# Optimization experiments

Hardware: AMD Instinct MI355X
Metric: run time of the kernel (lower is better)

The kernel has to match this reference:

```python
import jax, jax.numpy as jnp
import numpy as np

B = 4          # batch (number of point clouds)
NPER = 50000   # voxels per cloud
G = 96         # voxel grid extent per axis
C = 128        # in_channels
R = 2          # reduction_ratio
K = 27         # 3^3 kernel offsets
BN_EPS = 1e-5


def _build_sparse_geometry(seed=0):
    """Unique voxel coords per sample + 27-neighbor kernel map (Minkowski-style)."""
    rng = np.random.default_rng(seed)
    keys_list = []
    for b in range(B):
        loc = rng.choice(G ** 3, NPER, replace=False)
        loc.sort()
        keys_list.append(b * (G ** 3) + loc)
    keys = np.concatenate(keys_list)  # globally sorted (batch-major)
    N = keys.shape[0]
    loc = keys % (G ** 3)
    xs, ys, zs = loc // (G * G), (loc // G) % G, loc % G
    offsets = [(dx, dy, dz) for dx in (-1, 0, 1) for dy in (-1, 0, 1) for dz in (-1, 0, 1)]
    nbr_idx = np.zeros((N, K), np.int32)
    nbr_mask = np.zeros((N, K), bool)
    for k, (dx, dy, dz) in enumerate(offsets):
        inb = ((xs + dx >= 0) & (xs + dx < G) & (ys + dy >= 0) & (ys + dy < G)
               & (zs + dz >= 0) & (zs + dz < G))
        nkey = keys + dx * G * G + dy * G + dz
        pos = np.searchsorted(keys, nkey)
        pos_c = np.clip(pos, 0, N - 1)
        found = inb & (keys[pos_c] == nkey)
        nbr_idx[:, k] = np.where(found, pos_c, 0)
        nbr_mask[:, k] = found
    batch_idx = np.repeat(np.arange(B), NPER).astype(np.int32)
    return nbr_idx, nbr_mask, batch_idx


def setup_inputs() -> dict:
    nbr_idx, nbr_mask, batch_idx = _build_sparse_geometry(0)
    N = B * NPER
    key = jax.random.key(0)
    ks = jax.random.split(key, 8)
    feats = jax.random.normal(ks[0], (N, C), jnp.float32)
    # channel-attention MLP (MinkowskiLinear has bias=True)
    w1 = jax.random.normal(ks[1], (C, C // R), jnp.float32) * (1.0 / np.sqrt(C))
    b1 = jnp.zeros((C // R,), jnp.float32)
    w2 = jax.random.normal(ks[2], (C // R, C), jnp.float32) * (1.0 / np.sqrt(C // R))
    b2 = jnp.zeros((C,), jnp.float32)
    # spatial attention: 3x3x3 sparse conv C->4 (bias=False), BN(4), 1x1x1 conv 4->4
    conv1_w = jax.random.normal(ks[3], (K, C, 4), jnp.float32) * (1.0 / np.sqrt(K * C))
    bn_gamma = jnp.ones((4,), jnp.float32)
    bn_beta = jnp.zeros((4,), jnp.float32)
    conv2_w = jax.random.normal(ks[4], (4, 4), jnp.float32) * 0.5
    return dict(feats=feats, w1=w1, b1=b1, w2=w2, b2=b2, conv1_w=conv1_w,
                bn_gamma=bn_gamma, bn_beta=bn_beta, conv2_w=conv2_w,
                nbr_idx=jnp.asarray(nbr_idx), nbr_mask=jnp.asarray(nbr_mask),
                batch_idx=jnp.asarray(batch_idx), num_batches=B)


def reference(feats, w1, b1, w2, b2, conv1_w, bn_gamma, bn_beta, conv2_w,
              nbr_idx, nbr_mask, batch_idx, num_batches):
    N = feats.shape[0]
    ones = jnp.ones((N,), feats.dtype)
    counts = jax.ops.segment_sum(ones, batch_idx, num_segments=num_batches,
                                 indices_are_sorted=True)  # [B]
    avg_x = jax.ops.segment_sum(feats, batch_idx, num_segments=num_batches,
                                indices_are_sorted=True) / counts[:, None]  # [B,C]
    max_x = jax.ops.segment_max(feats, batch_idx, num_segments=num_batches,
                                indices_are_sorted=True)  # [B,C]
    mlp = lambda z: jax.nn.relu(z @ w1 + b1) @ w2 + b2
    weights = jax.nn.sigmoid(mlp(avg_x) + mlp(max_x))  # [B,C] channel attention
    # sam_mid: per-sample broadcast multiply
    mid = feats * weights[batch_idx]  # [N,C]
    # sparse 3x3x3 conv C->4 via kernel map (gather + thin matmul per offset)
    mask_f = nbr_mask.astype(feats.dtype)
    y = jnp.zeros((N, 4), feats.dtype)
    for k in range(K):
        y = y + (mid[nbr_idx[:, k]] * mask_f[:, k:k + 1]) @ conv1_w[k]
    # BatchNorm (training-mode batch stats, biased var) + ReLU
    mu = jnp.mean(y, axis=0)
    var = jnp.var(y, axis=0)
    y = (y - mu) * jax.lax.rsqrt(var + BN_EPS) * bn_gamma + bn_beta
    y = jax.nn.relu(y)
    # 1x1x1 conv == linear (bias=False), then sigmoid
    final = jax.nn.sigmoid(y @ conv2_w)  # [N,4]
    # sam_output: max over channels -> scalar spatial gate per point
    gate = jnp.max(final, axis=1, keepdims=True)  # [N,1]
    out = mid * gate + mid + feats
    return out
```

## Files before the change

kernel.cpp:

```cpp
#include <hip/hip_runtime.h>

#define C 128
#define K 27
#define BATCHES 4
#define RA_BPB 512
#define CONV_BLOCKS 512
#define CONV_TPB 1024
#define NWAVES_CONV (CONV_BLOCKS * (CONV_TPB / 64))
#define BN_EPS 1e-5f

typedef __attribute__((ext_vector_type(2))) __fp16 h2;
typedef __attribute__((ext_vector_type(8))) __fp16 h8;

__global__ __launch_bounds__(256) void reduceA_kernel(
    const float* __restrict__ feats, float* __restrict__ psum,
    float* __restrict__ pmax, const unsigned int* __restrict__ mwords,
    int* __restrict__ flag, int NPER) {
  int base = blockIdx.x * 512;
  bool bad = false;
  bad |= (mwords[base + threadIdx.x] > 1u);
  bad |= (mwords[base + 256 + threadIdx.x] > 1u);
  if (__any(bad) && (threadIdx.x & 63) == 0) atomicOr(flag, 1);

  int b = blockIdx.x / RA_BPB, chunk = blockIdx.x % RA_BPB;
  int CH = (NPER + RA_BPB - 1) / RA_BPB;
  int r0 = b * NPER + chunk * CH;
  int r1 = min(b * NPER + NPER, r0 + CH);
  int g = threadIdx.x >> 5;
  int l = threadIdx.x & 31;
  float4 s = make_float4(0.f, 0.f, 0.f, 0.f);
  float4 m = make_float4(-INFINITY, -INFINITY, -INFINITY, -INFINITY);
  int i = r0 + g;
  for (; i + 8 < r1; i += 16) {
    float4 v1 = *(const float4*)(feats + (size_t)i * C + l * 4);
    float4 v2 = *(const float4*)(feats + (size_t)(i + 8) * C + l * 4);
    s.x += v1.x + v2.x; s.y += v1.y + v2.y;
    s.z += v1.z + v2.z; s.w += v1.w + v2.w;
    m.x = fmaxf(m.x, fmaxf(v1.x, v2.x)); m.y = fmaxf(m.y, fmaxf(v1.y, v2.y));
    m.z = fmaxf(m.z, fmaxf(v1.z, v2.z)); m.w = fmaxf(m.w, fmaxf(v1.w, v2.w));
  }
  if (i < r1) {
    float4 v = *(const float4*)(feats + (size_t)i * C + l * 4);
    s.x += v.x; s.y += v.y; s.z += v.z; s.w += v.w;
    m.x = fmaxf(m.x, v.x); m.y = fmaxf(m.y, v.y);
    m.z = fmaxf(m.z, v.z); m.w = fmaxf(m.w, v.w);
  }
  __shared__ float ssum[8][C], smax[8][C];
  *(float4*)&ssum[g][l * 4] = s;
  *(float4*)&smax[g][l * 4] = m;
  __syncthreads();
  if (threadIdx.x < C) {
    int c = threadIdx.x;
    float S = 0.f, M = -INFINITY;
#pragma unroll
    for (int gg = 0; gg < 8; ++gg) {
      S += ssum[gg][c];
      M = fmaxf(M, smax[gg][c]);
    }
    psum[(size_t)blockIdx.x * C + c] = S;
    pmax[(size_t)blockIdx.x * C + c] = M;
  }
}

__global__ __launch_bounds__(256) void reduceB_kernel(
    const float* __restrict__ psum, const float* __restrict__ pmax,
    float* __restrict__ avg, float* __restrict__ mx, int NPER) {
  int b = blockIdx.x;
  int g = threadIdx.x >> 5, l = threadIdx.x & 31;
  float4 s = make_float4(0.f, 0.f, 0.f, 0.f);
  float4 m = make_float4(-INFINITY, -INFINITY, -INFINITY, -INFINITY);
  for (int j = g; j < RA_BPB; j += 8) {
    size_t base = (size_t)(b * RA_BPB + j) * C + l * 4;
    float4 vs = *(const float4*)(psum + base);
    float4 vm = *(const float4*)(pmax + base);
    s.x += vs.x; s.y += vs.y; s.z += vs.z; s.w += vs.w;
    m.x = fmaxf(m.x, vm.x); m.y = fmaxf(m.y, vm.y);
    m.z = fmaxf(m.z, vm.z); m.w = fmaxf(m.w, vm.w);
  }
  __shared__ float ssum[8][C], smax[8][C];
  *(float4*)&ssum[g][l * 4] = s;
  *(float4*)&smax[g][l * 4] = m;
  __syncthreads();
  if (threadIdx.x < C) {
    int c = threadIdx.x;
    float S = 0.f, M = -INFINITY;
#pragma unroll
    for (int gg = 0; gg < 8; ++gg) {
      S += ssum[gg][c];
      M = fmaxf(M, smax[gg][c]);
    }
    avg[b * C + c] = S / (float)NPER;
    mx[b * C + c] = M;
  }
}

__global__ void mlp_kernel(const float* __restrict__ avg, const float* __restrict__ mx,
                           const float* __restrict__ w1, const float* __restrict__ b1,
                           const float* __restrict__ w2, const float* __restrict__ b2,
                           float* __restrict__ wgt) {
  int b = blockIdx.x, t = threadIdx.x;
  __shared__ float h1a[64], h1m[64];
  if (t < 64) {
    float sa = b1[t], sm = b1[t];
    for (int c = 0; c < C; ++c) {
      float wv = w1[c * 64 + t];
      sa += avg[b * C + c] * wv;
      sm += mx[b * C + c] * wv;
    }
    h1a[t] = fmaxf(sa, 0.f);
    h1m[t] = fmaxf(sm, 0.f);
  }
  __syncthreads();
  float za = b2[t], zm = b2[t];
  for (int h = 0; h < 64; ++h) {
    float wv = w2[h * C + t];
    za += h1a[h] * wv;
    zm += h1m[h] * wv;
  }
  float z = za + zm;
  wgt[b * C + t] = 1.f / (1.f + expf(-z));
}

__global__ __launch_bounds__(CONV_TPB, 8) void conv_kernel(
    const float* __restrict__ feats, const float* __restrict__ wgt,
    const float* __restrict__ conv1_w, const int* __restrict__ nbr_idx,
    const void* __restrict__ nbr_mask, const int* __restrict__ flagp,
    float* __restrict__ y, float* __restrict__ bnpart, int N, int NPER) {
  __shared__ __align__(16) h8 wlds[K * 64];
  int tid = threadIdx.x;
  for (int e = tid; e < K * 64; e += CONV_TPB) {
    float4 A = ((const float4*)conv1_w)[e * 2];
    float4 B = ((const float4*)conv1_w)[e * 2 + 1];
    h8 w;
    h2 p;
    p = __builtin_amdgcn_cvt_pkrtz(A.x, B.x); w[0] = p[0]; w[1] = p[1];
    p = __builtin_amdgcn_cvt_pkrtz(A.y, B.y); w[2] = p[0]; w[3] = p[1];
    p = __builtin_amdgcn_cvt_pkrtz(A.z, B.z); w[4] = p[0]; w[5] = p[1];
    p = __builtin_amdgcn_cvt_pkrtz(A.w, B.w); w[6] = p[0]; w[7] = p[1];
    wlds[e] = w;
  }
  __syncthreads();

  int lane = tid & 63;
  int g = lane >> 4, cl = lane & 15;
  int gwave = blockIdx.x * (CONV_TPB / 64) + (tid >> 6);
  int nwaves = gridDim.x * (CONV_TPB / 64);
  int rpw = (N + nwaves - 1) / nwaves;
  int rbeg = gwave * rpw, rend = min(N, rbeg + rpw);
  bool byteMode = (*flagp != 0);
  const unsigned char* mb = (const unsigned char*)nbr_mask;
  const int* mi = (const int*)nbr_mask;

  int bB = min(rbeg / NPER, BATCHES - 1);
  int bEnd = (bB + 1) * NPER;
  float2 wr = *(const float2*)(wgt + bB * C + 2 * lane);

  bool mk = false;
  int jl = 0;
  if (rbeg < rend && lane < K) {
    size_t e = (size_t)rbeg * K + lane;
    mk = byteMode ? (mb[e] != 0) : (mi[e] != 0);
    jl = nbr_idx[e];
  }

  float sAcc = 0.f, qAcc = 0.f;

  unsigned balTailN = 0, balTailP = 0;
  int jN = 0, jP = 0, cntN = 0, cntP = 0;
  int k0N = 0, k1N = 0, k2N = 0, k3N = 0, k0P = 0, k1P = 0, k2P = 0, k3P = 0;
  float2 g0N = make_float2(0, 0), g1N = g0N, g2N = g0N, g3N = g0N;
  float2 g0P = g0N, g1P = g0N, g2P = g0N, g3P = g0N;

#define FRONT(iF)                                                           \
  do {                                                                      \
    unsigned bb = (unsigned)__ballot(mk);                                   \
    jN = jl;                                                                \
    mk = false;                                                             \
    if ((iF) + 1 < rend && lane < K) {                                      \
      size_t e = (size_t)((iF) + 1) * K + lane;                             \
      mk = byteMode ? (mb[e] != 0) : (mi[e] != 0);                          \
      jl = nbr_idx[e];                                                      \
    }                                                                       \
    cntN = __popc(bb);                                                      \
    k0N = __ffs(bb) - 1; bb &= bb - 1;                                      \
    k1N = __ffs(bb) - 1; bb &= bb - 1;                                      \
    k2N = __ffs(bb) - 1; bb &= bb - 1;                                      \
    k3N = __ffs(bb) - 1; bb &= bb - 1;                                      \
    balTailN = bb;                                                          \
    int j0 = __shfl(jN, k0N & 63);                                          \
    int j1 = __shfl(jN, k1N & 63);                                          \
    int j2 = __shfl(jN, k2N & 63);                                          \
    int j3 = __shfl(jN, k3N & 63);                                          \
    if (cntN > 0) g0N = *(const float2*)(feats + (size_t)j0 * C + 2 * lane);\
    if (cntN > 1) g1N = *(const float2*)(feats + (size_t)j1 * C + 2 * lane);\
    if (cntN > 2) g2N = *(const float2*)(feats + (size_t)j2 * C + 2 * lane);\
    if (cntN > 3) g3N = *(const float2*)(feats + (size_t)j3 * C + 2 * lane);\
  } while (0)

#define ACCD(ff, kk)                                                        \
  {                                                                         \
    h2 fp = __builtin_amdgcn_cvt_pkrtz(ff.x * wr.x, ff.y * wr.y);           \
    h8 w = wlds[(kk)*64 + lane];                                            \
    h2 w0 = __builtin_shufflevector(w, w, 0, 1);                            \
    h2 w1 = __builtin_shufflevector(w, w, 2, 3);                            \
    h2 w2 = __builtin_shufflevector(w, w, 4, 5);                            \
    h2 w3 = __builtin_shufflevector(w, w, 6, 7);                            \
    a0 = __builtin_amdgcn_fdot2(fp, w0, a0, false);                         \
    a1 = __builtin_amdgcn_fdot2(fp, w1, a1, false);                         \
    a2 = __builtin_amdgcn_fdot2(fp, w2, a2, false);                         \
    a3 = __builtin_amdgcn_fdot2(fp, w3, a3, false);                         \
  }

#define BACK(ir)                                                            \
  do {                                                                      \
    if ((ir) >= bEnd && bB < BATCHES - 1) {                                 \
      ++bB; bEnd += NPER;                                                   \
      wr = *(const float2*)(wgt + bB * C + 2 * lane);                       \
    }                                                                       \
    float a0 = 0, a1 = 0, a2 = 0, a3 = 0;                                   \
    if (cntP > 0) ACCD(g0P, k0P)                                            \
    if (cntP > 1) ACCD(g1P, k1P)                                            \
    if (cntP > 2) ACCD(g2P, k2P)                                            \
    if (cntP > 3) ACCD(g3P, k3P)                                            \
    unsigned bt = balTailP;                                                 \
    while (bt) {                                                            \
      int kk = __ffs(bt) - 1; bt &= bt - 1;                                 \
      int jj = __shfl(jP, kk);                                              \
      float2 f = *(const float2*)(feats + (size_t)jj * C + 2 * lane);       \
      ACCD(f, kk)                                                           \
    }                                                                       \
    a0 += __shfl_xor(a0, 16); a1 += __shfl_xor(a1, 16);                     \
    a2 += __shfl_xor(a2, 16); a3 += __shfl_xor(a3, 16);                     \
    a0 += __shfl_xor(a0, 32); a1 += __shfl_xor(a1, 32);                     \
    a2 += __shfl_xor(a2, 32); a3 += __shfl_xor(a3, 32);                     \
    float v = (g == 0) ? a0 : (g == 1) ? a1 : (g == 2) ? a2 : a3;           \
    v += __shfl_xor(v, 1);                                                  \
    v += __shfl_xor(v, 2);                                                  \
    v += __shfl_xor(v, 4);                                                  \
    v += __shfl_xor(v, 8);                                                  \
    if (cl == 0) y[(size_t)(ir)*4 + g] = v;                                 \
    sAcc += v; qAcc += v * v;                                               \
  } while (0)

#define ROTATE()                                                            \
  do {                                                                      \
    balTailP = balTailN; jP = jN; cntP = cntN;                              \
    k0P = k0N; k1P = k1N; k2P = k2N; k3P = k3N;                             \
    g0P = g0N; g1P = g1N; g2P = g2N; g3P = g3N;                             \
  } while (0)

  if (rbeg < rend) {
    FRONT(rbeg);
    ROTATE();
    for (int i = rbeg + 1; i < rend; ++i) {
      FRONT(i);
      BACK(i - 1);
      ROTATE();
    }
    BACK(rend - 1);
  }
#undef FRONT
#undef ACCD
#undef BACK
#undef ROTATE

  if (cl == 0) {
    float* p = bnpart + (size_t)gwave * 8;
    p[g] = sAcc;
    p[4 + g] = qAcc;
  }
}

__global__ void bn_reduce_kernel(const float* __restrict__ bnpart, int nparts,
                                 const float* __restrict__ gamma, const float* __restrict__ beta,
                                 float* __restrict__ scsh, int N) {
  __shared__ float red[256 * 8];
  int t = threadIdx.x;
  float S[8];
#pragma unroll
  for (int o = 0; o < 8; ++o) S[o] = 0.f;
  for (int i = t; i < nparts; i += 256) {
#pragma unroll
    for (int o = 0; o < 8; ++o) S[o] += bnpart[(size_t)i * 8 + o];
  }
#pragma unroll
  for (int o = 0; o < 8; ++o) red[t * 8 + o] = S[o];
  __syncthreads();
  for (int st = 128; st > 0; st >>= 1) {
    if (t < st) {
#pragma unroll
      for (int o = 0; o < 8; ++o) red[t * 8 + o] += red[(t + st) * 8 + o];
    }
    __syncthreads();
  }
  if (t == 0) {
    float invN = 1.f / (float)N;
#pragma unroll
    for (int o = 0; o < 4; ++o) {
      float mu = red[o] * invN;
      float var = red[4 + o] * invN - mu * mu;
      float sc = gamma[o] * rsqrtf(var + BN_EPS);
      scsh[o] = sc;
      scsh[4 + o] = beta[o] - mu * sc;
    }
  }
}

__global__ __launch_bounds__(256) void final_kernel(
    const float* __restrict__ feats, const float* __restrict__ wgt,
    const float* __restrict__ y, const float* __restrict__ scsh,
    const float* __restrict__ c2, float* __restrict__ out, int N, int NPER) {
  int lane = threadIdx.x & 63;
  int gwave = blockIdx.x * (blockDim.x >> 6) + (threadIdx.x >> 6);
  int nwaves = gridDim.x * (blockDim.x >> 6);
  int rpw = (N + nwaves - 1) / nwaves;
  int rbeg = gwave * rpw, rend = min(N, rbeg + rpw);
  if (rbeg >= rend) return;
  float4 sc = *(const float4*)scsh;
  float4 sh = *(const float4*)(scsh + 4);
  float4 r0 = *(const float4*)(c2 + 0);
  float4 r1 = *(const float4*)(c2 + 4);
  float4 r2 = *(const float4*)(c2 + 8);
  float4 r3 = *(const float4*)(c2 + 12);
  int bB = min(rbeg / NPER, BATCHES - 1);
  int bEnd = (bB + 1) * NPER;
  float2 w = *(const float2*)(wgt + bB * C + 2 * lane);

  float4 yvN = *(const float4*)(y + (size_t)rbeg * 4);
  float2 fN = *(const float2*)(feats + (size_t)rbeg * C + 2 * lane);
  for (int i = rbeg; i < rend; ++i) {
    float4 yv = yvN;
    float2 f = fN;
    if (i + 1 < rend) {
      yvN = *(const float4*)(y + (size_t)(i + 1) * 4);
      fN = *(const float2*)(feats + (size_t)(i + 1) * C + 2 * lane);
    }
    if (i >= bEnd && bB < BATCHES - 1) {
      ++bB; bEnd += NPER;
      w = *(const float2*)(wgt + bB * C + 2 * lane);
    }
    float y0 = fmaxf(yv.x * sc.x + sh.x, 0.f);
    float y1 = fmaxf(yv.y * sc.y + sh.y, 0.f);
    float y2 = fmaxf(yv.z * sc.z + sh.z, 0.f);
    float y3 = fmaxf(yv.w * sc.w + sh.w, 0.f);
    float z0 = y0 * r0.x + y1 * r1.x + y2 * r2.x + y3 * r3.x;
    float z1 = y0 * r0.y + y1 * r1.y + y2 * r2.y + y3 * r3.y;
    float z2 = y0 * r0.z + y1 * r1.z + y2 * r2.z + y3 * r3.z;
    float z3 = y0 * r0.w + y1 * r1.w + y2 * r2.w + y3 * r3.w;
    float zm = fmaxf(fmaxf(z0, z1), fmaxf(z2, z3));
    float gate = 1.f / (1.f + expf(-zm));
    float g1 = 1.f + gate;
    float2 o2;
    o2.x = f.x * (1.f + w.x * g1);
    o2.y = f.y * (1.f + w.y * g1);
    *(float2*)(out + (size_t)i * C + 2 * lane) = o2;
  }
}

extern "C" void kernel_launch(void* const* d_in, const int* in_sizes, int n_in,
                              void* d_out, int out_size, void* d_ws, size_t ws_size,
                              hipStream_t stream) {
  const float* feats   = (const float*)d_in[0];
  const float* w1      = (const float*)d_in[1];
  const float* b1      = (const float*)d_in[2];
  const float* w2      = (const float*)d_in[3];
  const float* b2      = (const float*)d_in[4];
  const float* conv1w  = (const float*)d_in[5];
  const float* gamma   = (const float*)d_in[6];
  const float* beta    = (const float*)d_in[7];
  const float* c2      = (const float*)d_in[8];
  const int*   nbr_idx = (const int*)d_in[9];
  const void*  nbr_mask = d_in[10];
  int N = in_sizes[0] / C;
  int NPER = N / BATCHES;

  char* ws = (char*)d_ws;
  size_t off = 0;
  int* flag = (int*)(ws + off);        off += 16;
  float* psum = (float*)(ws + off);    off += (size_t)BATCHES * RA_BPB * C * 4;
  float* pmax = (float*)(ws + off);    off += (size_t)BATCHES * RA_BPB * C * 4;
  float* avg  = (float*)(ws + off);    off += (size_t)BATCHES * C * 4;
  float* mx   = (float*)(ws + off);    off += (size_t)BATCHES * C * 4;
  float* wgt  = (float*)(ws + off);    off += (size_t)BATCHES * C * 4;
  float* y    = (float*)(ws + off);    off += (size_t)N * 4 * 4;
  float* bnpart = (float*)(ws + off);  off += (size_t)NWAVES_CONV * 8 * 4;
  float* scsh = (float*)(ws + off);    off += 64;
  float* outp = (float*)d_out;

  hipMemsetAsync(flag, 0, sizeof(int), stream);
  reduceA_kernel<<<BATCHES * RA_BPB, 256, 0, stream>>>(
      feats, psum, pmax, (const unsigned int*)nbr_mask, flag, NPER);
  reduceB_kernel<<<BATCHES, 256, 0, stream>>>(psum, pmax, avg, mx, NPER);
  mlp_kernel<<<BATCHES, C, 0, stream>>>(avg, mx, w1, b1, w2, b2, wgt);
  conv_kernel<<<CONV_BLOCKS, CONV_TPB, 0, stream>>>(feats, wgt, conv1w, nbr_idx, nbr_mask,
                                                    flag, y, bnpart, N, NPER);
  bn_reduce_kernel<<<1, 256, 0, stream>>>(bnpart, NWAVES_CONV, gamma, beta, scsh, N);
  final_kernel<<<2048, 256, 0, stream>>>(feats, wgt, y, scsh, c2, outp, N, NPER);
}
```

Before: 167.8 us.

## Process two rows per wave iteration in sparse conv and fuse reduceB with MLP

The conv kernel now has each wave handle two output rows per iteration. Both rows' 27 kernel-map entries load into 54 lanes, one 64-bit ballot covers them, and up to eight feature gathers are issued per step, which raises memory-level parallelism. The cross-lane reduction of the four accumulators is restructured to use fewer shuffles. The reduceB and MLP kernels are merged into one launch, with the averages kept in shared memory. The wider prefetch raises register pressure, and the batch-weight switch is now checked only at the first row of each pair, so a pair that straddles a batch boundary could use the wrong weights.

```diff
diff --git a/kernel.cpp b/kernel.cpp
--- a/kernel.cpp
+++ b/kernel.cpp
@@ -62,9 +62,11 @@
   }
 }
 
-__global__ __launch_bounds__(256) void reduceB_kernel(
+__global__ __launch_bounds__(256) void reduceB_mlp_kernel(
     const float* __restrict__ psum, const float* __restrict__ pmax,
-    float* __restrict__ avg, float* __restrict__ mx, int NPER) {
+    const float* __restrict__ w1, const float* __restrict__ b1,
+    const float* __restrict__ w2, const float* __restrict__ b2,
+    float* __restrict__ wgt, int NPER) {
   int b = blockIdx.x;
   int g = threadIdx.x >> 5, l = threadIdx.x & 31;
   float4 s = make_float4(0.f, 0.f, 0.f, 0.f);
@@ -81,6 +83,7 @@
   *(float4*)&ssum[g][l * 4] = s;
   *(float4*)&smax[g][l * 4] = m;
   __syncthreads();
+  __shared__ float avgs[C], mxs[C];
   if (threadIdx.x < C) {
     int c = threadIdx.x;
     float S = 0.f, M = -INFINITY;
@@ -89,36 +92,33 @@
       S += ssum[gg][c];
       M = fmaxf(M, smax[gg][c]);
     }
-    avg[b * C + c] = S / (float)NPER;
-    mx[b * C + c] = M;
-  }
-}
-
-__global__ void mlp_kernel(const float* __restrict__ avg, const float* __restrict__ mx,
-                           const float* __restrict__ w1, const float* __restrict__ b1,
-                           const float* __restrict__ w2, const float* __restrict__ b2,
-                           float* __restrict__ wgt) {
-  int b = blockIdx.x, t = threadIdx.x;
+    avgs[c] = S / (float)NPER;
+    mxs[c] = M;
+  }
+  __syncthreads();
   __shared__ float h1a[64], h1m[64];
+  int t = threadIdx.x;
   if (t < 64) {
     float sa = b1[t], sm = b1[t];
     for (int c = 0; c < C; ++c) {
       float wv = w1[c * 64 + t];
-      sa += avg[b * C + c] * wv;
-      sm += mx[b * C + c] * wv;
+      sa += avgs[c] * wv;
+      sm += mxs[c] * wv;
     }
     h1a[t] = fmaxf(sa, 0.f);
     h1m[t] = fmaxf(sm, 0.f);
   }
   __syncthreads();
-  float za = b2[t], zm = b2[t];
-  for (int h = 0; h < 64; ++h) {
-    float wv = w2[h * C + t];
-    za += h1a[h] * wv;
-    zm += h1m[h] * wv;
-  }
-  float z = za + zm;
-  wgt[b * C + t] = 1.f / (1.f + expf(-z));
+  if (t < C) {
+    float za = b2[t], zm = b2[t];
+    for (int h = 0; h < 64; ++h) {
+      float wv = w2[h * C + t];
+      za += h1a[h] * wv;
+      zm += h1m[h] * wv;
+    }
+    float z = za + zm;
+    wgt[b * C + t] = 1.f / (1.f + expf(-z));
+  }
 }
 
 __global__ __launch_bounds__(CONV_TPB, 8) void conv_kernel(
@@ -145,56 +145,81 @@
   int g = lane >> 4, cl = lane & 15;
   int gwave = blockIdx.x * (CONV_TPB / 64) + (tid >> 6);
   int nwaves = gridDim.x * (CONV_TPB / 64);
-  int rpw = (N + nwaves - 1) / nwaves;
-  int rbeg = gwave * rpw, rend = min(N, rbeg + rpw);
+  int Q = (N + 1) >> 1;
+  int qpw = (Q + nwaves - 1) / nwaves;
+  int qbeg = gwave * qpw, qend = min(Q, qbeg + qpw);
   bool byteMode = (*flagp != 0);
   const unsigned char* mb = (const unsigned char*)nbr_mask;
   const int* mi = (const int*)nbr_mask;
-
-  int bB = min(rbeg / NPER, BATCHES - 1);
+  long long maxE = (long long)N * K;
+
+  int bB = min((2 * qbeg) / NPER, BATCHES - 1);
   int bEnd = (bB + 1) * NPER;
   float2 wr = *(const float2*)(wgt + bB * C + 2 * lane);
 
   bool mk = false;
   int jl = 0;
-  if (rbeg < rend && lane < K) {
-    size_t e = (size_t)rbeg * K + lane;
-    mk = byteMode ? (mb[e] != 0) : (mi[e] != 0);
-    jl = nbr_idx[e];
+  if (qbeg < qend && lane < 2 * K) {
+    long long e = (long long)(2 * qbeg) * K + lane;
+    if (e < maxE) {
+      mk = byteMode ? (mb[e] != 0) : (mi[e] != 0);
+      jl = nbr_idx[e];
+    }
   }
 
   float sAcc = 0.f, qAcc = 0.f;
 
-  unsigned balTailN = 0, balTailP = 0;
-  int jN = 0, jP = 0, cntN = 0, cntP = 0;
-  int k0N = 0, k1N = 0, k2N = 0, k3N = 0, k0P = 0, k1P = 0, k2P = 0, k3P = 0;
-  float2 g0N = make_float2(0, 0), g1N = g0N, g2N = g0N, g3N = g0N;
-  float2 g0P = g0N, g1P = g0N, g2P = g0N, g3P = g0N;
-
-#define FRONT(iF)                                                           \
+  int jN = 0, jP = 0;
+  unsigned tailAN = 0, tailBN = 0, tailAP = 0, tailBP = 0;
+  int cntAN = 0, cntBN = 0, cntAP = 0, cntBP = 0;
+  int kA0N = 0, kA1N = 0, kA2N = 0, kA3N = 0, kB0N = 0, kB1N = 0, kB2N = 0, kB3N = 0;
+  int kA0P = 0, kA1P = 0, kA2P = 0, kA3P = 0, kB0P = 0, kB1P = 0, kB2P = 0, kB3P = 0;
+  float2 gA0N, gA1N, gA2N, gA3N, gB0N, gB1N, gB2N, gB3N;
+  float2 gA0P, gA1P, gA2P, gA3P, gB0P, gB1P, gB2P, gB3P;
+  gA0N = gA1N = gA2N = gA3N = gB0N = gB1N = gB2N = gB3N = make_float2(0.f, 0.f);
+  gA0P = gA1P = gA2P = gA3P = gB0P = gB1P = gB2P = gB3P = make_float2(0.f, 0.f);
+
+#define FRONT(qF)                                                           \
   do {                                                                      \
-    unsigned bb = (unsigned)__ballot(mk);                                   \
+    unsigned long long bb = __ballot(mk);                                   \
     jN = jl;                                                                \
     mk = false;                                                             \
-    if ((iF) + 1 < rend && lane < K) {                                      \
-      size_t e = (size_t)((iF) + 1) * K + lane;                             \
-      mk = byteMode ? (mb[e] != 0) : (mi[e] != 0);                          \
-      jl = nbr_idx[e];                                                      \
+    if ((qF) + 1 < qend && lane < 2 * K) {                                  \
+      long long e = (long long)(2 * ((qF) + 1)) * K + lane;                 \
+      if (e < maxE) {                                                       \
+        mk = byteMode ? (mb[e] != 0) : (mi[e] != 0);                        \
+        jl = nbr_idx[e];                                                    \
+      }                                                                     \
     }                                                                       \
-    cntN = __popc(bb);                                                      \
-    k0N = __ffs(bb) - 1; bb &= bb - 1;                                      \
-    k1N = __ffs(bb) - 1; bb &= bb - 1;                                      \
-    k2N = __ffs(bb) - 1; bb &= bb - 1;                                      \
-    k3N = __ffs(bb) - 1; bb &= bb - 1;                                      \
-    balTailN = bb;                                                          \
-    int j0 = __shfl(jN, k0N & 63);                                          \
-    int j1 = __shfl(jN, k1N & 63);                                          \
-    int j2 = __shfl(jN, k2N & 63);                                          \
-    int j3 = __shfl(jN, k3N & 63);                                          \
-    if (cntN > 0) g0N = *(const float2*)(feats + (size_t)j0 * C + 2 * lane);\
-    if (cntN > 1) g1N = *(const float2*)(feats + (size_t)j1 * C + 2 * lane);\
-    if (cntN > 2) g2N = *(const float2*)(feats + (size_t)j2 * C + 2 * lane);\
-    if (cntN > 3) g3N = *(const float2*)(feats + (size_t)j3 * C + 2 * lane);\
+    unsigned balA = (unsigned)(bb & 0x7FFFFFFull);                          \
+    unsigned balB = (unsigned)((bb >> 27) & 0x7FFFFFFull);                  \
+    cntAN = __popc(balA); cntBN = __popc(balB);                             \
+    kA0N = __ffs(balA) - 1; balA &= balA - 1;                               \
+    kA1N = __ffs(balA) - 1; balA &= balA - 1;                               \
+    kA2N = __ffs(balA) - 1; balA &= balA - 1;                               \
+    kA3N = __ffs(balA) - 1; balA &= balA - 1;                               \
+    tailAN = balA;                                                          \
+    kB0N = __ffs(balB) - 1; balB &= balB - 1;                               \
+    kB1N = __ffs(balB) - 1; balB &= balB - 1;                               \
+    kB2N = __ffs(balB) - 1; balB &= balB - 1;                               \
+    kB3N = __ffs(balB) - 1; balB &= balB - 1;                               \
+    tailBN = balB;                                                          \
+    int jA0 = __shfl(jN, kA0N & 63);                                        \
+    int jA1 = __shfl(jN, kA1N & 63);                                        \
+    int jA2 = __shfl(jN, kA2N & 63);                                        \
+    int jA3 = __shfl(jN, kA3N & 63);                                        \
+    int jB0 = __shfl(jN, (27 + kB0N) & 63);                                 \
+    int jB1 = __shfl(jN, (27 + kB1N) & 63);                                 \
+    int jB2 = __shfl(jN, (27 + kB2N) & 63);                                 \
+    int jB3 = __shfl(jN, (27 + kB3N) & 63);                                 \
+    if (cntAN > 0) gA0N = *(const float2*)(feats + (size_t)jA0 * C + 2 * lane); \
+    if (cntAN > 1) gA1N = *(const float2*)(feats + (size_t)jA1 * C + 2 * lane); \
+    if (cntAN > 2) gA2N = *(const float2*)(feats + (size_t)jA2 * C + 2 * lane); \
+    if (cntAN > 3) gA3N = *(const float2*)(feats + (size_t)jA3 * C + 2 * lane); \
+    if (cntBN > 0) gB0N = *(const float2*)(feats + (size_t)jB0 * C + 2 * lane); \
+    if (cntBN > 1) gB1N = *(const float2*)(feats + (size_t)jB1 * C + 2 * lane); \
+    if (cntBN > 2) gB2N = *(const float2*)(feats + (size_t)jB2 * C + 2 * lane); \
+    if (cntBN > 3) gB3N = *(const float2*)(feats + (size_t)jB3 * C + 2 * lane); \
   } while (0)
 
 #define ACCD(ff, kk)                                                        \
@@ -211,57 +236,77 @@
     a3 = __builtin_amdgcn_fdot2(fp, w3, a3, false);                         \
   }
 
-#define BACK(ir)                                                            \
+#define REDUCE_STORE(ir)                                                    \
   do {                                                                      \
-    if ((ir) >= bEnd && bB < BATCHES - 1) {                                 \
+    float u = (g < 2) ? a2 : a0;                                            \
+    float vv = (g < 2) ? a3 : a1;                                           \
+    float m0 = ((g < 2) ? a0 : a2) + __shfl_xor(u, 32);                     \
+    float m1 = ((g < 2) ? a1 : a3) + __shfl_xor(vv, 32);                    \
+    float w = (g & 1) ? m0 : m1;                                            \
+    float vf = ((g & 1) ? m1 : m0) + __shfl_xor(w, 16);                     \
+    vf += __shfl_xor(vf, 1);                                                \
+    vf += __shfl_xor(vf, 2);                                                \
+    vf += __shfl_xor(vf, 4);                                                \
+    vf += __shfl_xor(vf, 8);                                                \
+    if (cl == 0) y[(size_t)(ir)*4 + g] = vf;                                \
+    sAcc += vf; qAcc += vf * vf;                                            \
+  } while (0)
+
+#define BACKROW(cnt, K0, K1, K2, K3, TAIL, G0, G1, G2, G3, SOFF, ir)        \
+  do {                                                                      \
+    float a0 = 0, a1 = 0, a2 = 0, a3 = 0;                                   \
+    if (cnt > 0) ACCD(G0, K0)                                               \
+    if (cnt > 1) ACCD(G1, K1)                                               \
+    if (cnt > 2) ACCD(G2, K2)                                               \
+    if (cnt > 3) ACCD(G3, K3)                                               \
+    unsigned bt = TAIL;                                                     \
+    while (bt) {                                                            \
+      int kk = __ffs(bt) - 1; bt &= bt - 1;                                 \
+      int jj = __shfl(jP, (SOFF) + kk);                                     \
+      float2 f = *(const float2*)(feats + (size_t)jj * C + 2 * lane);       \
+      ACCD(f, kk)                                                           \
+    }                                                                       \
+    REDUCE_STORE(ir);                                                       \
+  } while (0)
+
+#define BACKPAIR(qr)                                                        \
+  do {                                                                      \
+    int rA = 2 * (qr);                                                      \
+    if (rA >= bEnd && bB < BATCHES - 1) {                                   \
       ++bB; bEnd += NPER;                                                   \
       wr = *(const float2*)(wgt + bB * C + 2 * lane);                       \
     }                                                                       \
-    float a0 = 0, a1 = 0, a2 = 0, a3 = 0;                                   \
-    if (cntP > 0) ACCD(g0P, k0P)                                            \
-    if (cntP > 1) ACCD(g1P, k1P)                                            \
-    if (cntP > 2) ACCD(g2P, k2P)                                            \
-    if (cntP > 3) ACCD(g3P, k3P)                                            \
-    unsigned bt = balTailP;                                                 \
-    while (bt) {                                                            \
-      int kk = __ffs(bt) - 1; bt &= bt - 1;                                 \
-      int jj = __shfl(jP, kk);                                              \
-      float2 f = *(const float2*)(feats + (size_t)jj * C + 2 * lane);       \
-      ACCD(f, kk)                                                           \
-    }                                                                       \
-    a0 += __shfl_xor(a0, 16); a1 += __shfl_xor(a1, 16);                     \
-    a2 += __shfl_xor(a2, 16); a3 += __shfl_xor(a3, 16);                     \
-    a0 += __shfl_xor(a0, 32); a1 += __shfl_xor(a1, 32);                     \
-    a2 += __shfl_xor(a2, 32); a3 += __shfl_xor(a3, 32);                     \
-    float v = (g == 0) ? a0 : (g == 1) ? a1 : (g == 2) ? a2 : a3;           \
-    v += __shfl_xor(v, 1);                                                  \
-    v += __shfl_xor(v, 2);                                                  \
-    v += __shfl_xor(v, 4);                                                  \
-    v += __shfl_xor(v, 8);                                                  \
-    if (cl == 0) y[(size_t)(ir)*4 + g] = v;                                 \
-    sAcc += v; qAcc += v * v;                                               \
+    BACKROW(cntAP, kA0P, kA1P, kA2P, kA3P, tailAP, gA0P, gA1P, gA2P, gA3P, 0, rA); \
+    if (rA + 1 < N)                                                         \
+      BACKROW(cntBP, kB0P, kB1P, kB2P, kB3P, tailBP, gB0P, gB1P, gB2P, gB3P, 27, rA + 1); \
   } while (0)
 
 #define ROTATE()                                                            \
   do {                                                                      \
-    balTailP = balTailN; jP = jN; cntP = cntN;                              \
-    k0P = k0N; k1P = k1N; k2P = k2N; k3P = k3N;                             \
-    g0P = g0N; g1P = g1N; g2P = g2N; g3P = g3N;                             \
+    jP = jN;                                                                \
+    tailAP = tailAN; tailBP = tailBN;                                       \
+    cntAP = cntAN; cntBP = cntBN;                                           \
+    kA0P = kA0N; kA1P = kA1N; kA2P = kA2N; kA3P = kA3N;                     \
+    kB0P = kB0N; kB1P = kB1N; kB2P = kB2N; kB3P = kB3N;                     \
+    gA0P = gA0N; gA1P = gA1N; gA2P = gA2N; gA3P = gA3N;                     \
+    gB0P = gB0N; gB1P = gB1N; gB2P = gB2N; gB3P = gB3N;                     \
   } while (0)
 
-  if (rbeg < rend) {
-    FRONT(rbeg);
+  if (qbeg < qend) {
+    FRONT(qbeg);
     ROTATE();
-    for (int i = rbeg + 1; i < rend; ++i) {
-      FRONT(i);
-      BACK(i - 1);
+    for (int q = qbeg + 1; q < qend; ++q) {
+      FRONT(q);
+      BACKPAIR(q - 1);
       ROTATE();
     }
-    BACK(rend - 1);
+    BACKPAIR(qend - 1);
   }
 #undef FRONT
 #undef ACCD
-#undef BACK
+#undef REDUCE_STORE
+#undef BACKROW
+#undef BACKPAIR
 #undef ROTATE
 
   if (cl == 0) {
@@ -379,8 +424,6 @@
   int* flag = (int*)(ws + off);        off += 16;
   float* psum = (float*)(ws + off);    off += (size_t)BATCHES * RA_BPB * C * 4;
   float* pmax = (float*)(ws + off);    off += (size_t)BATCHES * RA_BPB * C * 4;
-  float* avg  = (float*)(ws + off);    off += (size_t)BATCHES * C * 4;
-  float* mx   = (float*)(ws + off);    off += (size_t)BATCHES * C * 4;
   float* wgt  = (float*)(ws + off);    off += (size_t)BATCHES * C * 4;
   float* y    = (float*)(ws + off);    off += (size_t)N * 4 * 4;
   float* bnpart = (float*)(ws + off);  off += (size_t)NWAVES_CONV * 8 * 4;
@@ -390,8 +433,7 @@
   hipMemsetAsync(flag, 0, sizeof(int), stream);
   reduceA_kernel<<<BATCHES * RA_BPB, 256, 0, stream>>>(
       feats, psum, pmax, (const unsigned int*)nbr_mask, flag, NPER);
-  reduceB_kernel<<<BATCHES, 256, 0, stream>>>(psum, pmax, avg, mx, NPER);
-  mlp_kernel<<<BATCHES, C, 0, stream>>>(avg, mx, w1, b1, w2, b2, wgt);
+  reduceB_mlp_kernel<<<BATCHES, 256, 0, stream>>>(psum, pmax, w1, b1, w2, b2, wgt, NPER);
   conv_kernel<<<CONV_BLOCKS, CONV_TPB, 0, stream>>>(feats, wgt, conv1w, nbr_idx, nbr_mask,
                                                     flag, y, bnpart, N, NPER);
   bn_reduce_kernel<<<1, 256, 0, stream>>>(bnpart, NWAVES_CONV, gamma, beta, scsh, N);
```

After: 194.5 us. 1.16x slower.
